# Optimization experiments

Hardware: AMD Instinct MI355X
Metric: run time of the kernel (lower is better)

The kernel has to match this reference:

```python
import jax, jax.numpy as jnp
import numpy as np

B, T, F, C = 1024, 64, 1024, 3  # batch, num_trees, num_features, num_of_cls
NSLOT, N2 = 5, 16


def setup_inputs() -> dict:
    key = jax.random.key(0)
    ks = jax.random.split(key, 9)
    return {
        "d": jax.random.normal(ks[0], (B, 2048), jnp.float32),
        "idx": jax.random.randint(ks[1], (T, F), 0, 2048, jnp.int32),
        "cc": jax.random.randint(ks[2], (T, C), 0, NSLOT, jnp.int32),
        "w_clc": jax.random.normal(ks[3], (T, F, 2), jnp.float32) * 0.02,
        "b_clc": jax.random.normal(ks[4], (T, 2), jnp.float32) * 0.02,
        "w1": jax.random.normal(ks[5], (T, F, C), jnp.float32) * 0.02,
        "b1": jax.random.normal(ks[6], (T, C), jnp.float32) * 0.02,
        "w2": jax.random.normal(ks[7], (T, F + C, N2), jnp.float32) * 0.02,
        "b2": jax.random.normal(ks[8], (T, N2), jnp.float32) * 0.02,
    }


def reference(d, idx, cc, w_clc, b_clc, w1, b1, w2, b2):
    # Per-tree random feature gather: [B, T, F]
    g = d[:, idx]
    # Gate: clc[i](d[:, idx[i]]).log_softmax(-1)
    w = jax.nn.log_softmax(jnp.einsum('btf,tfc->btc', g, w_clc) + b_clc, axis=-1)
    # AgentCLS (eval mode: dropout = identity)
    logits1 = jnp.einsum('btf,tfc->btc', g, w1) + b1          # [B,T,C]
    y1 = jax.nn.log_softmax(logits1, axis=-1)
    x2 = jnp.concatenate([g, jax.nn.relu(logits1)], axis=-1)  # [B,T,F+C]
    y2 = jax.nn.log_softmax(jnp.einsum('btf,tfc->btc', x2, w2) + b2, axis=-1)
    # Gate-weighted scatter combine (get_output math)
    gate = jnp.exp(w[..., 1:2])                               # [B,T,1]
    onehot = jax.nn.one_hot(cc, NSLOT, dtype=d.dtype)         # [T,C,5]
    out5 = jnp.einsum('btc,tcx->bx', jnp.exp(y1) * gate, onehot)
    count5 = jnp.einsum('bt,tx->bx', gate[..., 0], onehot.sum(1))
    out5 = jnp.where(count5 > 0, out5 / jnp.where(count5 > 0, count5, 1.0), 0.0)
    gsum = gate.sum(1)                                        # [B,1]
    out16 = (jnp.exp(y2) * gate).sum(1) / gsum
    return jnp.concatenate([out5, out16], axis=-1)            # [B,21]
```

## Files before the change

kernel.cpp:

```cpp
#include <hip/hip_runtime.h>

#define NT 64
#define NF 1024
#define NB 1024
#define ND 2048
#define NTP 32
#define NN2 (NT * NTP)
#define NP 27
#define NW2ROW 1027
#define BK 64
#define BM 64
#define BN 64
#define NSCAT 2048
#define NCONV 1024

typedef __attribute__((ext_vector_type(8))) short short8;
typedef __attribute__((ext_vector_type(4))) float f32x4;

static __device__ __forceinline__ unsigned short f2bf(float x) {
    unsigned u = __float_as_uint(x);
    unsigned r = (u + 0x7FFFu + ((u >> 16) & 1u)) >> 16;
    return (unsigned short)r;
}

__global__ __launch_bounds__(256) void prep_kernel(
    const int* __restrict__ idx, const float* __restrict__ w_clc,
    const float* __restrict__ w1, const float* __restrict__ w2,
    const float* __restrict__ d, unsigned short* __restrict__ Wf,
    unsigned short* __restrict__ db)
{
    __shared__ float tile[ND];
    int bid = blockIdx.x;
    int tid = threadIdx.x;

    if (bid < NSCAT) {
        int t = bid >> 5, k = bid & 31;
        if (k >= 21) {
            uint4 z = make_uint4(0, 0, 0, 0);
            *(uint4*)&Wf[(size_t)bid * ND + tid * 8] = z;
            return;
        }
        for (int i = tid; i < ND; i += 256) tile[i] = 0.f;
        __syncthreads();

        const float* src; int stride;
        if (k < 2)      { src = w_clc + (size_t)t * 2048 + k;            stride = 2;  }
        else if (k < 5) { src = w1    + (size_t)t * 3072 + (k - 2);      stride = 3;  }
        else            { src = w2    + (size_t)t * NW2ROW * 16 + (k-5); stride = 16; }

        const int* idt = idx + t * NF;
        for (int f = tid; f < NF; f += 256)
            atomicAdd(&tile[idt[f]], src[(size_t)f * stride]);
        __syncthreads();

        int i8 = tid * 8;
        union { unsigned short u[8]; uint4 v; } pk;
#pragma unroll
        for (int e = 0; e < 8; ++e) pk.u[e] = f2bf(tile[i8 + e]);
        *(uint4*)&Wf[(size_t)bid * ND + i8] = pk.v;
    } else {
        int cb = bid - NSCAT;
        int i8 = (cb * 256 + tid) * 8;
        float4 a = *(const float4*)&d[i8];
        float4 b = *(const float4*)&d[i8 + 4];
        union { unsigned short u[8]; uint4 v; } pk;
        pk.u[0] = f2bf(a.x); pk.u[1] = f2bf(a.y); pk.u[2] = f2bf(a.z); pk.u[3] = f2bf(a.w);
        pk.u[4] = f2bf(b.x); pk.u[5] = f2bf(b.y); pk.u[6] = f2bf(b.z); pk.u[7] = f2bf(b.w);
        *(uint4*)&db[i8] = pk.v;
    }
}

__global__ __launch_bounds__(256, 2) void fused_kernel(
    const unsigned short* __restrict__ A,
    const unsigned short* __restrict__ Bm,
    const float* __restrict__ b_clc, const float* __restrict__ b1,
    const float* __restrict__ b2, const float* __restrict__ w2,
    const int* __restrict__ cc, float* __restrict__ ptl2)
{
    __shared__ __align__(16) char smem[32768];
    unsigned short (*As)[BM][BK] = (unsigned short(*)[BM][BK])smem;
    unsigned short (*Bs)[BN][BK] = (unsigned short(*)[BN][BK])(smem + 16384);
    float* Cl  = (float*)smem;
    float* red = (float*)(smem + 16896);

    int tid = threadIdx.x;
    int lane = tid & 63;
    int wv = tid >> 6;
    int wr = wv & 1;
    int wq = wv >> 1;
    int nb = blockIdx.x;
    int mb = blockIdx.y;
    int m0 = mb * BM;
    int n0 = nb * BN;
    int r0 = lane & 15;
    int kq = lane >> 4;
    int sx = r0 & 7;
    int sl0 = ((0 * 4 + kq) ^ sx) * 8;
    int sl1 = ((1 * 4 + kq) ^ sx) * 8;

    f32x4 acc[2][2];
#pragma unroll
    for (int mi = 0; mi < 2; ++mi)
#pragma unroll
        for (int ni = 0; ni < 2; ++ni) acc[mi][ni] = (f32x4)0.f;

#define STAGE(buf, kt)                                                          \
    {                                                                           \
        size_t koff = (size_t)(kt) * BK;                                        \
        _Pragma("unroll")                                                       \
        for (int p = 0; p < 2; ++p) {                                           \
            int chunk = p * 256 + tid;                                          \
            int row = chunk >> 3, c = chunk & 7;                                \
            int csw = (c ^ (row & 7)) * 8;                                      \
            const unsigned short* ga = A + (size_t)(m0 + row) * ND + koff + csw;\
            __builtin_amdgcn_global_load_lds(                                   \
                (const __attribute__((address_space(1))) void*)ga,              \
                (__attribute__((address_space(3))) void*)&As[buf][row][c * 8],  \
                16, 0, 0);                                                      \
        }                                                                       \
        _Pragma("unroll")                                                       \
        for (int p = 0; p < 2; ++p) {                                           \
            int chunk = p * 256 + tid;                                          \
            int row = chunk >> 3, c = chunk & 7;                                \
            int csw = (c ^ (row & 7)) * 8;                                      \
            const unsigned short* gb = Bm + (size_t)(n0 + row) * ND + koff + csw;\
            __builtin_amdgcn_global_load_lds(                                   \
                (const __attribute__((address_space(1))) void*)gb,              \
                (__attribute__((address_space(3))) void*)&Bs[buf][row][c * 8],  \
                16, 0, 0);                                                      \
        }                                                                       \
    }

    STAGE(0, 0);
    __syncthreads();

    int cur = 0;
    for (int kt = 0; kt < 32; ++kt) {
        if (kt < 31) STAGE(cur ^ 1, kt + 1);

        short8 af[2][2], bf[2][2];
#pragma unroll
        for (int mi = 0; mi < 2; ++mi) {
            af[mi][0] = *(const short8*)&As[cur][wr*32 + mi*16 + r0][sl0];
            af[mi][1] = *(const short8*)&As[cur][wr*32 + mi*16 + r0][sl1];
        }
#pragma unroll
        for (int ni = 0; ni < 2; ++ni) {
            bf[ni][0] = *(const short8*)&Bs[cur][wq*32 + ni*16 + r0][sl0];
            bf[ni][1] = *(const short8*)&Bs[cur][wq*32 + ni*16 + r0][sl1];
        }
#pragma unroll
        for (int ks = 0; ks < 2; ++ks)
#pragma unroll
            for (int mi = 0; mi < 2; ++mi)
#pragma unroll
                for (int ni = 0; ni < 2; ++ni)
                    acc[mi][ni] = __builtin_amdgcn_mfma_f32_16x16x32_bf16(
                        af[mi][ks], bf[ni][ks], acc[mi][ni], 0, 0, 0);
        __syncthreads();
        cur ^= 1;
    }
#undef STAGE

#pragma unroll
    for (int mi = 0; mi < 2; ++mi)
#pragma unroll
        for (int ni = 0; ni < 2; ++ni) {
            int n = wq * 32 + ni * 16 + r0;
            int bl = wr * 32 + mi * 16 + kq * 4;
#pragma unroll
            for (int q = 0; q < 4; ++q)
                Cl[(bl + q) * 65 + n] = acc[mi][ni][q];
        }
    __syncthreads();

    int tl = tid >> 6;
    int bl = lane;
    float s[NP];
#pragma unroll
    for (int k = 0; k < NP; ++k) s[k] = 0.f;

    if (tl < 2) {
        int t = nb * 2 + tl;

        float a21[21];
#pragma unroll
        for (int k = 0; k < 21; ++k) a21[k] = Cl[bl * 65 + tl * 32 + k];

        float L0 = a21[0] + b_clc[t * 2 + 0];
        float L1 = a21[1] + b_clc[t * 2 + 1];
        float mm = fmaxf(L0, L1);
        float e0 = __expf(L0 - mm), e1 = __expf(L1 - mm);
        float gate = e1 / (e0 + e1);

        float l1v[3];
        float m1 = -3.0e38f;
#pragma unroll
        for (int c = 0; c < 3; ++c) {
            l1v[c] = a21[2 + c] + b1[t * 3 + c];
            m1 = fmaxf(m1, l1v[c]);
        }
        float p1[3]; float S1 = 0.f;
#pragma unroll
        for (int c = 0; c < 3; ++c) { p1[c] = __expf(l1v[c] - m1); S1 += p1[c]; }
        float invS1g = gate / S1;

        float r0f = fmaxf(l1v[0], 0.f);
        float r1f = fmaxf(l1v[1], 0.f);
        float r2f = fmaxf(l1v[2], 0.f);

        const float* w2t = w2 + ((size_t)t * NW2ROW + NF) * 16;
        float l2[16]; float m2 = -3.0e38f;
#pragma unroll
        for (int nn = 0; nn < 16; ++nn) {
            float v = a21[5 + nn] + b2[t * 16 + nn];
            v = fmaf(r0f, w2t[nn], v);
            v = fmaf(r1f, w2t[16 + nn], v);
            v = fmaf(r2f, w2t[32 + nn], v);
            l2[nn] = v;
            m2 = fmaxf(m2, v);
        }
        float S2 = 0.f; float p2[16];
#pragma unroll
        for (int nn = 0; nn < 16; ++nn) { p2[nn] = __expf(l2[nn] - m2); S2 += p2[nn]; }
        float invS2g = gate * __frcp_rn(S2);

#pragma unroll
        for (int c = 0; c < 3; ++c) {
            int sl = cc[t * 3 + c];
            float pc = p1[c] * invS1g;
#pragma unroll
            for (int x = 0; x < 5; ++x) {
                if (sl == x) { s[x] += pc; s[5 + x] += gate; }
            }
        }
#pragma unroll
        for (int nn = 0; nn < 16; ++nn) s[10 + nn] += p2[nn] * invS2g;
        s[26] += gate;
    }

    if (tl == 1) {
#pragma unroll
        for (int k = 0; k < NP; ++k) red[k * 64 + bl] = s[k];
    }
    __syncthreads();
    if (tl != 0) return;

#pragma unroll
    for (int k = 0; k < NP; ++k) s[k] += red[k * 64 + bl];

    float* pt = ptl2 + (size_t)nb * NP * NB + m0 + bl;
#pragma unroll
    for (int k = 0; k < NP; ++k)
        pt[(size_t)k * NB] = s[k];
}

__global__ __launch_bounds__(256) void finalize_kernel(
    const float* __restrict__ ptl2, float* __restrict__ out)
{
    int lane = threadIdx.x & 63;
    int w = threadIdx.x >> 6;
    int b = blockIdx.x * 64 + lane;

    float s[NP];
#pragma unroll
    for (int k = 0; k < NP; ++k) s[k] = 0.f;
#pragma unroll
    for (int i = 0; i < 8; ++i) {
        const float* pt = ptl2 + (size_t)(w + i * 4) * NP * NB + b;
#pragma unroll
        for (int k = 0; k < NP; ++k) s[k] += pt[(size_t)k * NB];
    }

    __shared__ float red[3][NP][64];
    if (w > 0) {
#pragma unroll
        for (int k = 0; k < NP; ++k) red[w - 1][k][lane] = s[k];
    }
    __syncthreads();
    if (w != 0) return;
#pragma unroll
    for (int r = 0; r < 3; ++r)
#pragma unroll
        for (int k = 0; k < NP; ++k) s[k] += red[r][k][lane];

    float* ob = out + (size_t)b * 21;
#pragma unroll
    for (int x = 0; x < 5; ++x) {
        float c = s[5 + x];
        ob[x] = (c > 0.f) ? (s[x] / c) : 0.f;
    }
    float invg = 1.f / s[26];
#pragma unroll
    for (int n = 0; n < 16; ++n) ob[5 + n] = s[10 + n] * invg;
}

extern "C" void kernel_launch(void* const* d_in, const int* in_sizes, int n_in,
                              void* d_out, int out_size, void* d_ws, size_t ws_size,
                              hipStream_t stream)
{
    const float* d     = (const float*)d_in[0];
    const int*   idx   = (const int*)  d_in[1];
    const int*   cc    = (const int*)  d_in[2];
    const float* w_clc = (const float*)d_in[3];
    const float* b_clc = (const float*)d_in[4];
    const float* w1    = (const float*)d_in[5];
    const float* b1    = (const float*)d_in[6];
    const float* w2    = (const float*)d_in[7];
    const float* b2    = (const float*)d_in[8];
    float* out = (float*)d_out;

    unsigned short* Wf = (unsigned short*)d_ws;
    unsigned short* db = Wf + (size_t)NN2 * ND;
    float* ptl2 = (float*)(db + (size_t)NB * ND);

    prep_kernel<<<NSCAT + NCONV, 256, 0, stream>>>(idx, w_clc, w1, w2, d, Wf, db);
    fused_kernel<<<dim3(32, 16), 256, 0, stream>>>(db, Wf, b_clc, b1, b2, w2, cc, ptl2);
    finalize_kernel<<<16, 256, 0, stream>>>(ptl2, out);
}
```

Before: 44.22 us.

## Group weight-scatter columns per block and widen finalize reduction

```diff
diff --git a/kernel.cpp b/kernel.cpp
--- a/kernel.cpp
+++ b/kernel.cpp
@@ -11,8 +11,12 @@
 #define BK 64
 #define BM 64
 #define BN 64
-#define NSCAT 2048
+#define NKG 6
+#define NSCAT (NT * NKG)
+#define NPADROW (NT * 11)
+#define NPADBLK (NPADROW / 4)
 #define NCONV 1024
+#define PREP_GRID (NSCAT + NPADBLK + NCONV)
 
 typedef __attribute__((ext_vector_type(8))) short short8;
 typedef __attribute__((ext_vector_type(4))) float f32x4;
@@ -29,37 +33,58 @@
     const float* __restrict__ d, unsigned short* __restrict__ Wf,
     unsigned short* __restrict__ db)
 {
-    __shared__ float tile[ND];
+    __shared__ __align__(16) float tile[ND * 5];
     int bid = blockIdx.x;
     int tid = threadIdx.x;
 
     if (bid < NSCAT) {
-        int t = bid >> 5, k = bid & 31;
-        if (k >= 21) {
-            uint4 z = make_uint4(0, 0, 0, 0);
-            *(uint4*)&Wf[(size_t)bid * ND + tid * 8] = z;
-            return;
-        }
-        for (int i = tid; i < ND; i += 256) tile[i] = 0.f;
+        int t = bid / NKG, kg = bid % NKG;
+        int kbase = (kg == 0) ? 0 : (kg == 1) ? 2 : 5 + 4 * (kg - 2);
+        int kw    = (kg == 0) ? 2 : (kg == 1) ? 3 : 4;
+
+        float4* tz = (float4*)tile;
+        for (int i = tid; i < ND * 5 / 4; i += 256) tz[i] = make_float4(0, 0, 0, 0);
         __syncthreads();
 
-        const float* src; int stride;
-        if (k < 2)      { src = w_clc + (size_t)t * 2048 + k;            stride = 2;  }
-        else if (k < 5) { src = w1    + (size_t)t * 3072 + (k - 2);      stride = 3;  }
-        else            { src = w2    + (size_t)t * NW2ROW * 16 + (k-5); stride = 16; }
-
         const int* idt = idx + t * NF;
-        for (int f = tid; f < NF; f += 256)
-            atomicAdd(&tile[idt[f]], src[(size_t)f * stride]);
+#pragma unroll
+        for (int it = 0; it < 4; ++it) {
+            int f = it * 256 + tid;
+            int j = idt[f];
+            float v[4];
+            if (kg == 0) {
+                float2 a = *(const float2*)&w_clc[(size_t)(t * NF + f) * 2];
+                v[0] = a.x; v[1] = a.y;
+            } else if (kg == 1) {
+                const float* p = &w1[(size_t)(t * NF + f) * 3];
+                v[0] = p[0]; v[1] = p[1]; v[2] = p[2];
+            } else {
+                float4 a = *(const float4*)&w2[((size_t)t * NW2ROW + f) * 16 + (kg - 2) * 4];
+                v[0] = a.x; v[1] = a.y; v[2] = a.z; v[3] = a.w;
+            }
+            for (int c = 0; c < kw; ++c)
+                atomicAdd(&tile[j * 5 + c], v[c]);
+        }
         __syncthreads();
 
-        int i8 = tid * 8;
-        union { unsigned short u[8]; uint4 v; } pk;
-#pragma unroll
-        for (int e = 0; e < 8; ++e) pk.u[e] = f2bf(tile[i8 + e]);
-        *(uint4*)&Wf[(size_t)bid * ND + i8] = pk.v;
+        int j0 = tid * 8;
+        for (int c = 0; c < kw; ++c) {
+            union { unsigned short u[8]; uint4 v; } pk;
+#pragma unroll
+            for (int e = 0; e < 8; ++e) pk.u[e] = f2bf(tile[(j0 + e) * 5 + c]);
+            *(uint4*)&Wf[(size_t)(t * NTP + kbase + c) * ND + j0] = pk.v;
+        }
+    } else if (bid < NSCAT + NPADBLK) {
+        int pb = bid - NSCAT;
+        uint4 z = make_uint4(0, 0, 0, 0);
+#pragma unroll
+        for (int q = 0; q < 4; ++q) {
+            int r = pb * 4 + q;
+            int t = r / 11, k = 21 + r % 11;
+            *(uint4*)&Wf[(size_t)(t * NTP + k) * ND + tid * 8] = z;
+        }
     } else {
-        int cb = bid - NSCAT;
+        int cb = bid - NSCAT - NPADBLK;
         int i8 = (cb * 256 + tid) * 8;
         float4 a = *(const float4*)&d[i8];
         float4 b = *(const float4*)&d[i8 + 4];
@@ -255,9 +280,10 @@
         pt[(size_t)k * NB] = s[k];
 }
 
-__global__ __launch_bounds__(256) void finalize_kernel(
+__global__ __launch_bounds__(1024) void finalize_kernel(
     const float* __restrict__ ptl2, float* __restrict__ out)
 {
+    __shared__ float red[8][NP][64];
     int lane = threadIdx.x & 63;
     int w = threadIdx.x >> 6;
     int b = blockIdx.x * 64 + lane;
@@ -266,23 +292,50 @@
 #pragma unroll
     for (int k = 0; k < NP; ++k) s[k] = 0.f;
 #pragma unroll
-    for (int i = 0; i < 8; ++i) {
-        const float* pt = ptl2 + (size_t)(w + i * 4) * NP * NB + b;
+    for (int i = 0; i < 2; ++i) {
+        const float* pt = ptl2 + (size_t)(w * 2 + i) * NP * NB + b;
 #pragma unroll
         for (int k = 0; k < NP; ++k) s[k] += pt[(size_t)k * NB];
     }
 
-    __shared__ float red[3][NP][64];
-    if (w > 0) {
-#pragma unroll
-        for (int k = 0; k < NP; ++k) red[w - 1][k][lane] = s[k];
+    if (w >= 8) {
+#pragma unroll
+        for (int k = 0; k < NP; ++k) red[w - 8][k][lane] = s[k];
+    }
+    __syncthreads();
+    if (w < 8) {
+#pragma unroll
+        for (int k = 0; k < NP; ++k) s[k] += red[w][k][lane];
+    }
+    __syncthreads();
+    if (w >= 4 && w < 8) {
+#pragma unroll
+        for (int k = 0; k < NP; ++k) red[w - 4][k][lane] = s[k];
+    }
+    __syncthreads();
+    if (w < 4) {
+#pragma unroll
+        for (int k = 0; k < NP; ++k) s[k] += red[w][k][lane];
+    }
+    __syncthreads();
+    if (w >= 2 && w < 4) {
+#pragma unroll
+        for (int k = 0; k < NP; ++k) red[w - 2][k][lane] = s[k];
+    }
+    __syncthreads();
+    if (w < 2) {
+#pragma unroll
+        for (int k = 0; k < NP; ++k) s[k] += red[w][k][lane];
+    }
+    __syncthreads();
+    if (w == 1) {
+#pragma unroll
+        for (int k = 0; k < NP; ++k) red[0][k][lane] = s[k];
     }
     __syncthreads();
     if (w != 0) return;
 #pragma unroll
-    for (int r = 0; r < 3; ++r)
-#pragma unroll
-        for (int k = 0; k < NP; ++k) s[k] += red[r][k][lane];
+    for (int k = 0; k < NP; ++k) s[k] += red[0][k][lane];
 
     float* ob = out + (size_t)b * 21;
 #pragma unroll
@@ -314,7 +367,7 @@
     unsigned short* db = Wf + (size_t)NN2 * ND;
     float* ptl2 = (float*)(db + (size_t)NB * ND);
 
-    prep_kernel<<<NSCAT + NCONV, 256, 0, stream>>>(idx, w_clc, w1, w2, d, Wf, db);
+    prep_kernel<<<PREP_GRID, 256, 0, stream>>>(idx, w_clc, w1, w2, d, Wf, db);
     fused_kernel<<<dim3(32, 16), 256, 0, stream>>>(db, Wf, b_clc, b1, b2, w2, cc, ptl2);
-    finalize_kernel<<<16, 256, 0, stream>>>(ptl2, out);
-}
+    finalize_kernel<<<16, 1024, 0, stream>>>(ptl2, out);
+}
```

Measured after the change: 47.28 us. 6.9% more time.
